# Performance work log

Hardware: AMD Instinct MI355X
Metric: run time of the kernel (lower is better)

The kernel has to match this reference:

```python
import jax, jax.numpy as jnp
import numpy as np

N = 4096
IN_F = 256
OUT_F = 128
K = 3
BETA = 0.5
ALPHA = 0.2  # leaky relu negative slope
NEG_BIG = -9e15


def setup_inputs() -> dict:
    key = jax.random.key(0)
    k1, k2, k3, k4 = jax.random.split(key, 4)
    h = jax.random.normal(k1, (N, IN_F), dtype=jnp.float32)
    k_mask_list = jax.random.randint(k2, (K, N, N), 0, 2, dtype=jnp.int32)
    # xavier_uniform with gain=1.414
    def xavier(k, shape, gain=1.414):
        fan_in, fan_out = shape[0], shape[1]
        bound = gain * np.sqrt(6.0 / (fan_in + fan_out))
        return jax.random.uniform(k, shape, jnp.float32, -bound, bound)
    W = xavier(k3, (IN_F * K, OUT_F))
    a = xavier(k4, (2 * OUT_F * K, 1))
    return {"h": h, "k_mask_list": k_mask_list, "W": W, "a": a}


def reference(h, k_mask_list, W, a):
    # dropout p=0.0 / eval mode -> identity
    Wh = None
    for i in range(K - 1, -1, -1):
        Whnew = h @ W[i * IN_F:(i + 1) * IN_F, :]              # [N, OUT_F]
        if i == K - 1:
            Wh = Whnew
        a1 = a[2 * i * OUT_F:(2 * i + 1) * OUT_F, :]           # [OUT_F, 1]
        a2 = a[(2 * i + 1) * OUT_F:(2 * i + 2) * OUT_F, :]     # [OUT_F, 1]
        Wh1 = Whnew @ a1                                        # [N, 1]
        Wh2 = Whnew @ a2                                        # [N, 1]
        e = jax.nn.leaky_relu(Wh1 + Wh2.T, negative_slope=ALPHA)  # [N, N]
        masked = jnp.where(k_mask_list[i] > 0, e, NEG_BIG)
        attention = jax.nn.softmax(masked, axis=1)              # [N, N]
        Wh = (1.0 - BETA) * (attention @ Whnew) + BETA * Wh
    return jax.nn.elu(Wh)  # concat=True
```

## Files before the change

kernel.cpp:

```cpp
#include <hip/hip_runtime.h>
#include <hip/hip_bf16.h>

#define NN 4096
#define IN_F 256
#define OUT_F 128
#define ALPHA 0.2f

typedef __bf16 bf16x8 __attribute__((ext_vector_type(8)));
typedef float f32x4 __attribute__((ext_vector_type(4)));
typedef float f32x16 __attribute__((ext_vector_type(16)));

__device__ __forceinline__ float bf2f(unsigned short u) {
  return __uint_as_float(((unsigned int)u) << 16);
}
__device__ __forceinline__ unsigned short f2bf(float f) {
  union { float f; unsigned int u; } x; x.f = f;
  unsigned int r = x.u + 0x7FFF + ((x.u >> 16) & 1);
  return (unsigned short)(r >> 16);
}
__device__ __forceinline__ bf16x8 bits2bf8(unsigned int b) {
  union { unsigned int u[4]; bf16x8 v; } o;
  #pragma unroll
  for (int e = 0; e < 4; ++e) {
    unsigned int lo = (b >> (2 * e)) & 1u;
    unsigned int hi = (b >> (2 * e + 1)) & 1u;
    o.u[e] = lo * 0x3F80u + hi * 0x3F800000u;
  }
  return o.v;
}

__global__ __launch_bounds__(256) void k_cvt_w(const float* __restrict__ W,
                                               unsigned short* __restrict__ Wtb) {
  const int i = blockIdx.y;
  const int k0 = blockIdx.x * 32;
  const int t = threadIdx.x;
  __shared__ float tile[32][129];
  #pragma unroll
  for (int j = 0; j < 16; ++j) {
    int idx = t + j * 256;
    int r = idx >> 7, c = idx & 127;
    tile[r][c] = W[(size_t)(i * IN_F + k0 + r) * OUT_F + c];
  }
  __syncthreads();
  const int c = t >> 1, half = t & 1;
  unsigned short* dst = Wtb + ((size_t)i * OUT_F + c) * IN_F + k0 + half * 16;
  #pragma unroll
  for (int g = 0; g < 4; ++g) {
    ushort4 v;
    v.x = f2bf(tile[half * 16 + g * 4 + 0][c]);
    v.y = f2bf(tile[half * 16 + g * 4 + 1][c]);
    v.z = f2bf(tile[half * 16 + g * 4 + 2][c]);
    v.w = f2bf(tile[half * 16 + g * 4 + 3][c]);
    *(ushort4*)(dst + g * 4) = v;
  }
}

__global__ __launch_bounds__(256) void k_front(const float* __restrict__ h,
                                               const unsigned short* __restrict__ Wtb,
                                               const float* __restrict__ a,
                                               float* __restrict__ Whnewf,
                                               float* __restrict__ Wh1,
                                               float* __restrict__ Wh2) {
  const int i = blockIdx.y;
  const int r0 = blockIdx.x * 32;
  const int t = threadIdx.x;
  const int lane = t & 63, wid = t >> 6;
  const int m = wid & 1, nh = wid >> 1, nbase = nh * 64;
  const int ln = lane & 15, lk = lane >> 4;

  __shared__ float a1s[128], a2s[128];
  __shared__ float red1[2][32], red2[2][32];

  if (t < 128) {
    a1s[t] = a[(size_t)2 * i * OUT_F + t];
    a2s[t] = a[(size_t)(2 * i + 1) * OUT_F + t];
  }
  __syncthreads();

  const float* ap = h + (size_t)(r0 + m * 16 + ln) * IN_F + lk * 8;
  const unsigned short* bp = Wtb + ((size_t)i * OUT_F + nbase + ln) * IN_F + lk * 8;

  f32x4 z4 = {0.f, 0.f, 0.f, 0.f};
  f32x4 acc[4] = {z4, z4, z4, z4};
  #pragma unroll
  for (int ks = 0; ks < 8; ++ks) {
    float4 h0 = *(const float4*)(ap + ks * 32);
    float4 h1 = *(const float4*)(ap + ks * 32 + 4);
    union { unsigned short u[8]; bf16x8 v; } av;
    av.u[0] = f2bf(h0.x); av.u[1] = f2bf(h0.y); av.u[2] = f2bf(h0.z); av.u[3] = f2bf(h0.w);
    av.u[4] = f2bf(h1.x); av.u[5] = f2bf(h1.y); av.u[6] = f2bf(h1.z); av.u[7] = f2bf(h1.w);
    acc[0] = __builtin_amdgcn_mfma_f32_16x16x32_bf16(av.v, *(const bf16x8*)(bp + 0 * 16 * IN_F + ks * 32), acc[0], 0, 0, 0);
    acc[1] = __builtin_amdgcn_mfma_f32_16x16x32_bf16(av.v, *(const bf16x8*)(bp + 1 * 16 * IN_F + ks * 32), acc[1], 0, 0, 0);
    acc[2] = __builtin_amdgcn_mfma_f32_16x16x32_bf16(av.v, *(const bf16x8*)(bp + 2 * 16 * IN_F + ks * 32), acc[2], 0, 0, 0);
    acc[3] = __builtin_amdgcn_mfma_f32_16x16x32_bf16(av.v, *(const bf16x8*)(bp + 3 * 16 * IN_F + ks * 32), acc[3], 0, 0, 0);
  }

  float d1[4] = {0.f, 0.f, 0.f, 0.f}, d2[4] = {0.f, 0.f, 0.f, 0.f};
  #pragma unroll
  for (int f = 0; f < 4; ++f) {
    const int col = nbase + f * 16 + ln;
    const float va1 = a1s[col], va2 = a2s[col];
    #pragma unroll
    for (int q = 0; q < 4; ++q) {
      const int row = m * 16 + lk * 4 + q;
      const float v = acc[f][q];
      Whnewf[((size_t)i * NN + r0 + row) * OUT_F + col] = v;
      d1[q] += v * va1;
      d2[q] += v * va2;
    }
  }
  #pragma unroll
  for (int msk = 1; msk < 16; msk <<= 1) {
    #pragma unroll
    for (int q = 0; q < 4; ++q) {
      d1[q] += __shfl_xor(d1[q], msk, 64);
      d2[q] += __shfl_xor(d2[q], msk, 64);
    }
  }
  if (ln == 0) {
    #pragma unroll
    for (int q = 0; q < 4; ++q) {
      red1[nh][m * 16 + lk * 4 + q] = d1[q];
      red2[nh][m * 16 + lk * 4 + q] = d2[q];
    }
  }
  __syncthreads();
  if (t < 32) {
    Wh1[(size_t)i * NN + r0 + t] = red1[0][t] + red1[1][t];
    Wh2[(size_t)i * NN + r0 + t] = red2[0][t] + red2[1][t];
  }
}

__global__ __launch_bounds__(256) void k_gp(const float* __restrict__ Wh1,
                                            const float* __restrict__ Wh2,
                                            unsigned short* __restrict__ ew2pb,
                                            unsigned short* __restrict__ ew2mb,
                                            float* __restrict__ fpv,
                                            float* __restrict__ fmv) {
  const int i = blockIdx.x;
  const int t = threadIdx.x;
  __shared__ float red[4];
  __shared__ float gshared;
  float w2l[16];
  float m = -3.0e38f;
  #pragma unroll
  for (int j = 0; j < 16; ++j) {
    w2l[j] = Wh2[(size_t)i * NN + t + j * 256];
    m = fmaxf(m, w2l[j]);
  }
  #pragma unroll
  for (int o = 32; o > 0; o >>= 1) m = fmaxf(m, __shfl_down(m, o, 64));
  if ((t & 63) == 0) red[t >> 6] = m;
  __syncthreads();
  if (t == 0) gshared = fmaxf(fmaxf(red[0], red[1]), fmaxf(red[2], red[3]));
  __syncthreads();
  const float gi = gshared;
  #pragma unroll
  for (int j = 0; j < 16; ++j) {
    const int id = (int)((size_t)i * NN) + t + j * 256;
    ew2pb[id] = f2bf(__expf(w2l[j]));
    ew2mb[id] = f2bf(__expf(ALPHA * w2l[j]));
    float w1 = Wh1[id];
    float e0 = w1 + gi;
    float mx = (e0 > 0.f) ? e0 : ALPHA * e0;
    fpv[id] = __expf(w1 - mx);
    fmv[id] = __expf(ALPHA * w1 - mx);
  }
}

__global__ __launch_bounds__(256) void k_scale(const float* __restrict__ Whnewf,
                                               const unsigned short* __restrict__ ew2pb,
                                               const unsigned short* __restrict__ ew2mb,
                                               unsigned short* __restrict__ Vopt) {
  const int i = blockIdx.y;
  const int k0 = blockIdx.x * 32;
  const int t = threadIdx.x;
  __shared__ float tile[32][129];
  __shared__ float ewsp[32], ewsm[32];
  if (t < 32) {
    ewsp[t] = bf2f(ew2pb[(size_t)i * NN + k0 + t]);
    ewsm[t] = bf2f(ew2mb[(size_t)i * NN + k0 + t]);
  }
  #pragma unroll
  for (int j = 0; j < 16; ++j) {
    int idx = t + j * 256;
    int r = idx >> 7, c = idx & 127;
    tile[r][c] = Whnewf[((size_t)i * NN + k0 + r) * OUT_F + c];
  }
  __syncthreads();
  const int n = t & 127, ks = t >> 7;
  const int kslab = (k0 >> 4) + ks;
  #pragma unroll
  for (int s = 0; s < 2; ++s) {
    const float* ew = (s == 0) ? ewsp : ewsm;
    union { unsigned short u[16]; uint4 q[2]; } o;
    #pragma unroll
    for (int j = 0; j < 16; ++j) {
      const int cl = ks * 16 + j;
      o.u[j] = f2bf(ew[cl] * tile[cl][n]);
    }
    unsigned short* dst = Vopt + (((size_t)(i * 2 + s) * 256 + kslab) * 128 + n) * 16;
    *(uint4*)(dst) = o.q[0];
    *(uint4*)(dst + 8) = o.q[1];
  }
}

__global__ __launch_bounds__(256) void k_bits(const int* __restrict__ mask,
                                              const float* __restrict__ Wh1,
                                              const float* __restrict__ Wh2,
                                              unsigned int* __restrict__ Bits) {
  const int t = threadIdx.x;
  const int i = blockIdx.x >> 10;
  const int r0 = (blockIdx.x & 1023) * 4;
  float w2v[16];
  #pragma unroll
  for (int g = 0; g < 4; ++g) {
    float4 w2 = *(const float4*)(Wh2 + (size_t)i * NN + t * 16 + g * 4);
    w2v[g * 4 + 0] = w2.x; w2v[g * 4 + 1] = w2.y;
    w2v[g * 4 + 2] = w2.z; w2v[g * 4 + 3] = w2.w;
  }
  float w1v[4];
  #pragma unroll
  for (int rr = 0; rr < 4; ++rr) w1v[rr] = Wh1[(size_t)i * NN + r0 + rr];
  const int* mbase = mask + ((size_t)i * NN + r0) * NN + t * 16;
  int mA[16], mB[16];
  auto LD = [&](int rr, int* mv) {
    #pragma unroll
    for (int g = 0; g < 4; ++g) {
      int4 v = *(const int4*)(mbase + (size_t)rr * NN + g * 4);
      mv[g * 4 + 0] = v.x; mv[g * 4 + 1] = v.y;
      mv[g * 4 + 2] = v.z; mv[g * 4 + 3] = v.w;
    }
  };
  auto PR = [&](int rr, const int* mv) {
    const float w1 = w1v[rr];
    unsigned int bp = 0, bm = 0;
    #pragma unroll
    for (int j = 0; j < 16; ++j) {
      if (mv[j] > 0) {
        if (w1 + w2v[j] > 0.f) bp |= 1u << j; else bm |= 1u << j;
      }
    }
    Bits[((size_t)i * NN + r0 + rr) * 256 + t] = bp | (bm << 16);
  };
  LD(0, mA);
  LD(1, mB);
  PR(0, mA);
  LD(2, mA);
  PR(1, mB);
  LD(3, mB);
  PR(2, mA);
  PR(3, mB);
}

__global__ __launch_bounds__(256) void k_attn2(const unsigned short* __restrict__ Vopt,
                                               const unsigned int* __restrict__ Bits,
                                               const unsigned short* __restrict__ ew2pb,
                                               const unsigned short* __restrict__ ew2mb,
                                               const float* __restrict__ fpv,
                                               const float* __restrict__ fmv,
                                               float* __restrict__ Upart,
                                               float* __restrict__ SPp,
                                               float* __restrict__ SMp) {
  const unsigned int lid = blockIdx.x + 64u * (blockIdx.y + 3u * blockIdx.z);
  const unsigned int swz = (lid & 7u) * 96u + (lid >> 3);
  const int bx = swz & 63;
  const int w = swz >> 6;
  const int i = w % 3;
  const int z = w / 3;

  const int r0 = bx * 64;
  const int cb = z * 1024;
  const int t = threadIdx.x, lane = t & 63, wid = t >> 6;
  const int m = wid & 1, nh = wid >> 1;
  const int l31 = lane & 31, kh = lane >> 5;
  const int n0 = nh * 64 + l31, n1 = n0 + 32;

  const unsigned int* brow = Bits + ((size_t)i * NN + r0 + m * 32 + l31) * 256 + (cb >> 4);
  const size_t fragoff = (size_t)nh * 1024 + l31 * 16 + kh * 8;
  const unsigned short* vP = Vopt + ((size_t)(i * 2 + 0) * 256 + (cb >> 4)) * 2048 + fragoff;
  const unsigned short* vM = Vopt + ((size_t)(i * 2 + 1) * 256 + (cb >> 4)) * 2048 + fragoff;
  const unsigned short* eB = (nh == 0 ? ew2pb : ew2mb) + (size_t)i * NN + cb + kh * 8;

  f32x16 accP0 = {}, accP1 = {}, accM0 = {}, accM1 = {}, accS = {};

  #pragma unroll 2
  for (int chunk = 0; chunk < 16; ++chunk) {
    uint4 wv4 = *(const uint4*)(brow + chunk * 4);
    unsigned int wv[4] = {wv4.x, wv4.y, wv4.z, wv4.w};
    #pragma unroll
    for (int kst = 0; kst < 4; ++kst) {
      const int kslab = chunk * 4 + kst;
      unsigned int sh = wv[kst] >> (kh * 8);
      bf16x8 aP = bits2bf8(sh & 0xFFu);
      bf16x8 aM = bits2bf8((sh >> 16) & 0xFFu);
      bf16x8 bP0 = *(const bf16x8*)(vP + (size_t)kslab * 2048);
      bf16x8 bP1 = *(const bf16x8*)(vP + (size_t)kslab * 2048 + 512);
      bf16x8 bM0 = *(const bf16x8*)(vM + (size_t)kslab * 2048);
      bf16x8 bM1 = *(const bf16x8*)(vM + (size_t)kslab * 2048 + 512);
      bf16x8 eF  = *(const bf16x8*)(eB + kslab * 16);
      accP0 = __builtin_amdgcn_mfma_f32_32x32x16_bf16(aP, bP0, accP0, 0, 0, 0);
      accP1 = __builtin_amdgcn_mfma_f32_32x32x16_bf16(aP, bP1, accP1, 0, 0, 0);
      accM0 = __builtin_amdgcn_mfma_f32_32x32x16_bf16(aM, bM0, accM0, 0, 0, 0);
      accM1 = __builtin_amdgcn_mfma_f32_32x32x16_bf16(aM, bM1, accM1, 0, 0, 0);
      accS  = __builtin_amdgcn_mfma_f32_32x32x16_bf16(nh == 0 ? aP : aM, eF, accS, 0, 0, 0);
    }
  }

  const int rbase = r0 + m * 32;
  #pragma unroll
  for (int q = 0; q < 16; ++q) {
    const int crow = (q & 3) + 8 * (q >> 2) + 4 * kh;
    const int r = rbase + crow;
    const float fp = fpv[(size_t)i * NN + r];
    const float fm = fmv[(size_t)i * NN + r];
    float* urow = Upart + ((size_t)(z * 3 + i) * NN + r) * OUT_F;
    urow[n0] = fp * accP0[q] + fm * accM0[q];
    urow[n1] = fp * accP1[q] + fm * accM1[q];
  }
  if (l31 == 0) {
    #pragma unroll
    for (int q = 0; q < 16; ++q) {
      const int r = rbase + (q & 3) + 8 * (q >> 2) + 4 * kh;
      if (nh == 0) SPp[(size_t)(z * 3 + i) * NN + r] = accS[q];
      else         SMp[(size_t)(z * 3 + i) * NN + r] = accS[q];
    }
  }
}

__global__ __launch_bounds__(256) void k_final(const float* __restrict__ Upart,
                                               const float* __restrict__ SPp,
                                               const float* __restrict__ SMp,
                                               const float* __restrict__ fpv,
                                               const float* __restrict__ fmv,
                                               const float* __restrict__ Whnewf,
                                               float* __restrict__ out) {
  int idx = blockIdx.x * 256 + threadIdx.x;
  int r = idx >> 7;
  float v = 0.125f * Whnewf[(size_t)2 * NN * OUT_F + idx];
  #pragma unroll
  for (int i = 0; i < 3; ++i) {
    const float coef = (i == 0) ? 0.5f : (i == 1) ? 0.25f : 0.125f;
    float u = 0.f, sp = 0.f, sm = 0.f;
    #pragma unroll
    for (int zz = 0; zz < 4; ++zz) {
      u  += Upart[((size_t)(zz * 3 + i) * NN) * OUT_F + idx];
      sp += SPp[(size_t)(zz * 3 + i) * NN + r];
      sm += SMp[(size_t)(zz * 3 + i) * NN + r];
    }
    const float S = fpv[(size_t)i * NN + r] * sp + fmv[(size_t)i * NN + r] * sm;
    v += coef * u / S;
  }
  out[idx] = (v > 0.f) ? v : (__expf(v) - 1.0f);
}

extern "C" void kernel_launch(void* const* d_in, const int* in_sizes, int n_in,
                              void* d_out, int out_size, void* d_ws, size_t ws_size,
                              hipStream_t stream) {
  const float* h    = (const float*)d_in[0];
  const int*   mask = (const int*)d_in[1];
  const float* W    = (const float*)d_in[2];
  const float* a    = (const float*)d_in[3];
  float* out = (float*)d_out;

  float* Whnewf = (float*)d_ws;
  float* Wh1    = Whnewf + (size_t)3 * NN * OUT_F;
  float* Wh2    = Wh1 + 3 * NN;
  float* fpv    = Wh2 + 3 * NN;
  float* fmv    = fpv + 3 * NN;
  float* Upart  = fmv + 3 * NN;
  float* SPp    = Upart + (size_t)4 * 3 * NN * OUT_F;
  float* SMp    = SPp + 4 * 3 * NN;
  unsigned short* Wtb   = (unsigned short*)(SMp + 4 * 3 * NN);
  unsigned short* Vopt  = Wtb + (size_t)3 * OUT_F * IN_F;
  unsigned short* ew2pb = Vopt + (size_t)3 * 2 * 256 * 128 * 16;
  unsigned short* ew2mb = ew2pb + 3 * NN;
  unsigned int*   Bits  = (unsigned int*)(ew2mb + 3 * NN);

  k_cvt_w<<<dim3(8, 3), 256, 0, stream>>>(W, Wtb);
  k_front<<<dim3(128, 3), 256, 0, stream>>>(h, Wtb, a, Whnewf, Wh1, Wh2);
  k_gp<<<3, 256, 0, stream>>>(Wh1, Wh2, ew2pb, ew2mb, fpv, fmv);
  k_scale<<<dim3(128, 3), 256, 0, stream>>>(Whnewf, ew2pb, ew2mb, Vopt);
  k_bits<<<3072, 256, 0, stream>>>(mask, Wh1, Wh2, Bits);
  k_attn2<<<dim3(64, 3, 4), 256, 0, stream>>>(Vopt, Bits, ew2pb, ew2mb, fpv, fmv, Upart, SPp, SMp);
  k_final<<<(NN * OUT_F) / 256, 256, 0, stream>>>(Upart, SPp, SMp, fpv, fmv, Whnewf, out);
}
```

Measured before the change: 360.1 us.

## Fuse mask bit-packing into attention kernel and fold exp/scale prep into front GEMM

Removes the separate k_gp, k_scale and k_bits kernels. The attention kernel now reads the int32 mask and Wh2 directly and builds the bf16 selector operands in-loop. The front GEMM kernel now computes the exp(Wh2) factors and writes the scaled bf16 V tiles from LDS, using an atomicMax for the per-head max shift. The fp/fm factors are recomputed on the fly in the consumers instead of being stored. This cuts launches and intermediate buffer round-trips, but the heavy kernel's inner loop now carries wide mask loads and compare logic that may expose memory latency. The positive-only atomicMax also changes the softmax shift when the max is negative, which cancels mathematically.

```diff
diff --git a/kernel.cpp b/kernel.cpp
--- a/kernel.cpp
+++ b/kernel.cpp
@@ -10,23 +10,10 @@
 typedef float f32x4 __attribute__((ext_vector_type(4)));
 typedef float f32x16 __attribute__((ext_vector_type(16)));
 
-__device__ __forceinline__ float bf2f(unsigned short u) {
-  return __uint_as_float(((unsigned int)u) << 16);
-}
 __device__ __forceinline__ unsigned short f2bf(float f) {
   union { float f; unsigned int u; } x; x.f = f;
   unsigned int r = x.u + 0x7FFF + ((x.u >> 16) & 1);
   return (unsigned short)(r >> 16);
-}
-__device__ __forceinline__ bf16x8 bits2bf8(unsigned int b) {
-  union { unsigned int u[4]; bf16x8 v; } o;
-  #pragma unroll
-  for (int e = 0; e < 4; ++e) {
-    unsigned int lo = (b >> (2 * e)) & 1u;
-    unsigned int hi = (b >> (2 * e + 1)) & 1u;
-    o.u[e] = lo * 0x3F80u + hi * 0x3F800000u;
-  }
-  return o.v;
 }
 
 __global__ __launch_bounds__(256) void k_cvt_w(const float* __restrict__ W,
@@ -58,9 +45,13 @@
 __global__ __launch_bounds__(256) void k_front(const float* __restrict__ h,
                                                const unsigned short* __restrict__ Wtb,
                                                const float* __restrict__ a,
-                                               float* __restrict__ Whnewf,
+                                               float* __restrict__ Whnew2,
+                                               unsigned short* __restrict__ Vopt,
                                                float* __restrict__ Wh1,
-                                               float* __restrict__ Wh2) {
+                                               float* __restrict__ Wh2,
+                                               unsigned short* __restrict__ ew2pb,
+                                               unsigned short* __restrict__ ew2mb,
+                                               float* __restrict__ gmax2) {
   const int i = blockIdx.y;
   const int r0 = blockIdx.x * 32;
   const int t = threadIdx.x;
@@ -70,6 +61,8 @@
 
   __shared__ float a1s[128], a2s[128];
   __shared__ float red1[2][32], red2[2][32];
+  __shared__ float ewsp[32], ewsm[32];
+  __shared__ unsigned short T[2][32][130];
 
   if (t < 128) {
     a1s[t] = a[(size_t)2 * i * OUT_F + t];
@@ -102,9 +95,7 @@
     const float va1 = a1s[col], va2 = a2s[col];
     #pragma unroll
     for (int q = 0; q < 4; ++q) {
-      const int row = m * 16 + lk * 4 + q;
       const float v = acc[f][q];
-      Whnewf[((size_t)i * NN + r0 + row) * OUT_F + col] = v;
       d1[q] += v * va1;
       d2[q] += v * va2;
     }
@@ -124,141 +115,67 @@
       red2[nh][m * 16 + lk * 4 + q] = d2[q];
     }
   }
-  __syncthreads();
+  if (i == 2) {
+    #pragma unroll
+    for (int f = 0; f < 4; ++f) {
+      const int col = nbase + f * 16 + ln;
+      #pragma unroll
+      for (int q = 0; q < 4; ++q)
+        Whnew2[(size_t)(r0 + m * 16 + lk * 4 + q) * OUT_F + col] = acc[f][q];
+    }
+  }
+  __syncthreads();
+
   if (t < 32) {
-    Wh1[(size_t)i * NN + r0 + t] = red1[0][t] + red1[1][t];
-    Wh2[(size_t)i * NN + r0 + t] = red2[0][t] + red2[1][t];
-  }
-}
-
-__global__ __launch_bounds__(256) void k_gp(const float* __restrict__ Wh1,
-                                            const float* __restrict__ Wh2,
-                                            unsigned short* __restrict__ ew2pb,
-                                            unsigned short* __restrict__ ew2mb,
-                                            float* __restrict__ fpv,
-                                            float* __restrict__ fmv) {
-  const int i = blockIdx.x;
-  const int t = threadIdx.x;
-  __shared__ float red[4];
-  __shared__ float gshared;
-  float w2l[16];
-  float m = -3.0e38f;
-  #pragma unroll
-  for (int j = 0; j < 16; ++j) {
-    w2l[j] = Wh2[(size_t)i * NN + t + j * 256];
-    m = fmaxf(m, w2l[j]);
-  }
-  #pragma unroll
-  for (int o = 32; o > 0; o >>= 1) m = fmaxf(m, __shfl_down(m, o, 64));
-  if ((t & 63) == 0) red[t >> 6] = m;
-  __syncthreads();
-  if (t == 0) gshared = fmaxf(fmaxf(red[0], red[1]), fmaxf(red[2], red[3]));
-  __syncthreads();
-  const float gi = gshared;
-  #pragma unroll
-  for (int j = 0; j < 16; ++j) {
-    const int id = (int)((size_t)i * NN) + t + j * 256;
-    ew2pb[id] = f2bf(__expf(w2l[j]));
-    ew2mb[id] = f2bf(__expf(ALPHA * w2l[j]));
-    float w1 = Wh1[id];
-    float e0 = w1 + gi;
-    float mx = (e0 > 0.f) ? e0 : ALPHA * e0;
-    fpv[id] = __expf(w1 - mx);
-    fmv[id] = __expf(ALPHA * w1 - mx);
-  }
-}
-
-__global__ __launch_bounds__(256) void k_scale(const float* __restrict__ Whnewf,
-                                               const unsigned short* __restrict__ ew2pb,
-                                               const unsigned short* __restrict__ ew2mb,
-                                               unsigned short* __restrict__ Vopt) {
-  const int i = blockIdx.y;
-  const int k0 = blockIdx.x * 32;
-  const int t = threadIdx.x;
-  __shared__ float tile[32][129];
-  __shared__ float ewsp[32], ewsm[32];
-  if (t < 32) {
-    ewsp[t] = bf2f(ew2pb[(size_t)i * NN + k0 + t]);
-    ewsm[t] = bf2f(ew2mb[(size_t)i * NN + k0 + t]);
-  }
-  #pragma unroll
-  for (int j = 0; j < 16; ++j) {
-    int idx = t + j * 256;
-    int r = idx >> 7, c = idx & 127;
-    tile[r][c] = Whnewf[((size_t)i * NN + k0 + r) * OUT_F + c];
-  }
-  __syncthreads();
+    const float w1 = red1[0][t] + red1[1][t];
+    const float w2 = red2[0][t] + red2[1][t];
+    Wh1[(size_t)i * NN + r0 + t] = w1;
+    Wh2[(size_t)i * NN + r0 + t] = w2;
+    const float ep = __expf(w2), em = __expf(ALPHA * w2);
+    ewsp[t] = ep; ewsm[t] = em;
+    ew2pb[(size_t)i * NN + r0 + t] = f2bf(ep);
+    ew2mb[(size_t)i * NN + r0 + t] = f2bf(em);
+    float mv = w2;
+    #pragma unroll
+    for (int o = 16; o > 0; o >>= 1) mv = fmaxf(mv, __shfl_down(mv, o, 32));
+    if (t == 0 && mv > 0.f)
+      atomicMax((int*)gmax2 + i, __float_as_int(mv));
+  }
+  __syncthreads();
+
+  #pragma unroll
+  for (int f = 0; f < 4; ++f) {
+    const int n = nbase + f * 16 + ln;
+    #pragma unroll
+    for (int q = 0; q < 4; ++q) {
+      const int c = m * 16 + lk * 4 + q;
+      const float v = acc[f][q];
+      T[0][c][n] = f2bf(ewsp[c] * v);
+      T[1][c][n] = f2bf(ewsm[c] * v);
+    }
+  }
+  __syncthreads();
+
   const int n = t & 127, ks = t >> 7;
-  const int kslab = (k0 >> 4) + ks;
+  const int kslab = (r0 >> 4) + ks;
   #pragma unroll
   for (int s = 0; s < 2; ++s) {
-    const float* ew = (s == 0) ? ewsp : ewsm;
     union { unsigned short u[16]; uint4 q[2]; } o;
     #pragma unroll
-    for (int j = 0; j < 16; ++j) {
-      const int cl = ks * 16 + j;
-      o.u[j] = f2bf(ew[cl] * tile[cl][n]);
-    }
+    for (int j = 0; j < 16; ++j) o.u[j] = T[s][ks * 16 + j][n];
     unsigned short* dst = Vopt + (((size_t)(i * 2 + s) * 256 + kslab) * 128 + n) * 16;
     *(uint4*)(dst) = o.q[0];
     *(uint4*)(dst + 8) = o.q[1];
   }
 }
 
-__global__ __launch_bounds__(256) void k_bits(const int* __restrict__ mask,
-                                              const float* __restrict__ Wh1,
-                                              const float* __restrict__ Wh2,
-                                              unsigned int* __restrict__ Bits) {
-  const int t = threadIdx.x;
-  const int i = blockIdx.x >> 10;
-  const int r0 = (blockIdx.x & 1023) * 4;
-  float w2v[16];
-  #pragma unroll
-  for (int g = 0; g < 4; ++g) {
-    float4 w2 = *(const float4*)(Wh2 + (size_t)i * NN + t * 16 + g * 4);
-    w2v[g * 4 + 0] = w2.x; w2v[g * 4 + 1] = w2.y;
-    w2v[g * 4 + 2] = w2.z; w2v[g * 4 + 3] = w2.w;
-  }
-  float w1v[4];
-  #pragma unroll
-  for (int rr = 0; rr < 4; ++rr) w1v[rr] = Wh1[(size_t)i * NN + r0 + rr];
-  const int* mbase = mask + ((size_t)i * NN + r0) * NN + t * 16;
-  int mA[16], mB[16];
-  auto LD = [&](int rr, int* mv) {
-    #pragma unroll
-    for (int g = 0; g < 4; ++g) {
-      int4 v = *(const int4*)(mbase + (size_t)rr * NN + g * 4);
-      mv[g * 4 + 0] = v.x; mv[g * 4 + 1] = v.y;
-      mv[g * 4 + 2] = v.z; mv[g * 4 + 3] = v.w;
-    }
-  };
-  auto PR = [&](int rr, const int* mv) {
-    const float w1 = w1v[rr];
-    unsigned int bp = 0, bm = 0;
-    #pragma unroll
-    for (int j = 0; j < 16; ++j) {
-      if (mv[j] > 0) {
-        if (w1 + w2v[j] > 0.f) bp |= 1u << j; else bm |= 1u << j;
-      }
-    }
-    Bits[((size_t)i * NN + r0 + rr) * 256 + t] = bp | (bm << 16);
-  };
-  LD(0, mA);
-  LD(1, mB);
-  PR(0, mA);
-  LD(2, mA);
-  PR(1, mB);
-  LD(3, mB);
-  PR(2, mA);
-  PR(3, mB);
-}
-
-__global__ __launch_bounds__(256) void k_attn2(const unsigned short* __restrict__ Vopt,
-                                               const unsigned int* __restrict__ Bits,
+__global__ __launch_bounds__(256) void k_heavy(const unsigned short* __restrict__ Vopt,
+                                               const int* __restrict__ mask,
+                                               const float* __restrict__ Wh1,
+                                               const float* __restrict__ Wh2,
                                                const unsigned short* __restrict__ ew2pb,
                                                const unsigned short* __restrict__ ew2mb,
-                                               const float* __restrict__ fpv,
-                                               const float* __restrict__ fmv,
+                                               const float* __restrict__ gmax2,
                                                float* __restrict__ Upart,
                                                float* __restrict__ SPp,
                                                float* __restrict__ SMp) {
@@ -276,7 +193,11 @@
   const int l31 = lane & 31, kh = lane >> 5;
   const int n0 = nh * 64 + l31, n1 = n0 + 32;
 
-  const unsigned int* brow = Bits + ((size_t)i * NN + r0 + m * 32 + l31) * 256 + (cb >> 4);
+  const int myrow = r0 + m * 32 + l31;
+  const float w1 = Wh1[(size_t)i * NN + myrow];
+  const int* mrow = mask + ((size_t)i * NN + myrow) * NN + cb + kh * 8;
+  const float* w2p = Wh2 + (size_t)i * NN + cb + kh * 8;
+
   const size_t fragoff = (size_t)nh * 1024 + l31 * 16 + kh * 8;
   const unsigned short* vP = Vopt + ((size_t)(i * 2 + 0) * 256 + (cb >> 4)) * 2048 + fragoff;
   const unsigned short* vM = Vopt + ((size_t)(i * 2 + 1) * 256 + (cb >> 4)) * 2048 + fragoff;
@@ -285,35 +206,48 @@
   f32x16 accP0 = {}, accP1 = {}, accM0 = {}, accM1 = {}, accS = {};
 
   #pragma unroll 2
-  for (int chunk = 0; chunk < 16; ++chunk) {
-    uint4 wv4 = *(const uint4*)(brow + chunk * 4);
-    unsigned int wv[4] = {wv4.x, wv4.y, wv4.z, wv4.w};
-    #pragma unroll
-    for (int kst = 0; kst < 4; ++kst) {
-      const int kslab = chunk * 4 + kst;
-      unsigned int sh = wv[kst] >> (kh * 8);
-      bf16x8 aP = bits2bf8(sh & 0xFFu);
-      bf16x8 aM = bits2bf8((sh >> 16) & 0xFFu);
-      bf16x8 bP0 = *(const bf16x8*)(vP + (size_t)kslab * 2048);
-      bf16x8 bP1 = *(const bf16x8*)(vP + (size_t)kslab * 2048 + 512);
-      bf16x8 bM0 = *(const bf16x8*)(vM + (size_t)kslab * 2048);
-      bf16x8 bM1 = *(const bf16x8*)(vM + (size_t)kslab * 2048 + 512);
-      bf16x8 eF  = *(const bf16x8*)(eB + kslab * 16);
-      accP0 = __builtin_amdgcn_mfma_f32_32x32x16_bf16(aP, bP0, accP0, 0, 0, 0);
-      accP1 = __builtin_amdgcn_mfma_f32_32x32x16_bf16(aP, bP1, accP1, 0, 0, 0);
-      accM0 = __builtin_amdgcn_mfma_f32_32x32x16_bf16(aM, bM0, accM0, 0, 0, 0);
-      accM1 = __builtin_amdgcn_mfma_f32_32x32x16_bf16(aM, bM1, accM1, 0, 0, 0);
-      accS  = __builtin_amdgcn_mfma_f32_32x32x16_bf16(nh == 0 ? aP : aM, eF, accS, 0, 0, 0);
-    }
-  }
-
+  for (int kslab = 0; kslab < 64; ++kslab) {
+    const int ks16 = kslab * 16;
+    int4 ma = *(const int4*)(mrow + ks16);
+    int4 mb = *(const int4*)(mrow + ks16 + 4);
+    float4 wa = *(const float4*)(w2p + ks16);
+    float4 wb = *(const float4*)(w2p + ks16 + 4);
+
+    union { unsigned int u[4]; bf16x8 v; } aP, aM;
+    {
+      int mv[8] = {ma.x, ma.y, ma.z, ma.w, mb.x, mb.y, mb.z, mb.w};
+      float wv[8] = {wa.x, wa.y, wa.z, wa.w, wb.x, wb.y, wb.z, wb.w};
+      #pragma unroll
+      for (int e = 0; e < 4; ++e) {
+        const bool m0 = mv[2 * e] > 0,   p0 = (w1 + wv[2 * e]) > 0.f;
+        const bool m1 = mv[2 * e + 1] > 0, p1 = (w1 + wv[2 * e + 1]) > 0.f;
+        aP.u[e] = ((m0 && p0) ? 0x3F80u : 0u) | ((m1 && p1) ? 0x3F800000u : 0u);
+        aM.u[e] = ((m0 && !p0) ? 0x3F80u : 0u) | ((m1 && !p1) ? 0x3F800000u : 0u);
+      }
+    }
+    bf16x8 bP0 = *(const bf16x8*)(vP + (size_t)kslab * 2048);
+    bf16x8 bP1 = *(const bf16x8*)(vP + (size_t)kslab * 2048 + 512);
+    bf16x8 bM0 = *(const bf16x8*)(vM + (size_t)kslab * 2048);
+    bf16x8 bM1 = *(const bf16x8*)(vM + (size_t)kslab * 2048 + 512);
+    bf16x8 eF  = *(const bf16x8*)(eB + ks16);
+    accP0 = __builtin_amdgcn_mfma_f32_32x32x16_bf16(aP.v, bP0, accP0, 0, 0, 0);
+    accP1 = __builtin_amdgcn_mfma_f32_32x32x16_bf16(aP.v, bP1, accP1, 0, 0, 0);
+    accM0 = __builtin_amdgcn_mfma_f32_32x32x16_bf16(aM.v, bM0, accM0, 0, 0, 0);
+    accM1 = __builtin_amdgcn_mfma_f32_32x32x16_bf16(aM.v, bM1, accM1, 0, 0, 0);
+    accS  = __builtin_amdgcn_mfma_f32_32x32x16_bf16(nh == 0 ? aP.v : aM.v, eF, accS, 0, 0, 0);
+  }
+
+  const float gi = gmax2[i];
   const int rbase = r0 + m * 32;
   #pragma unroll
   for (int q = 0; q < 16; ++q) {
     const int crow = (q & 3) + 8 * (q >> 2) + 4 * kh;
     const int r = rbase + crow;
-    const float fp = fpv[(size_t)i * NN + r];
-    const float fm = fmv[(size_t)i * NN + r];
+    const float rw1 = Wh1[(size_t)i * NN + r];
+    const float e0 = rw1 + gi;
+    const float mx = (e0 > 0.f) ? e0 : ALPHA * e0;
+    const float fp = __expf(rw1 - mx);
+    const float fm = __expf(ALPHA * rw1 - mx);
     float* urow = Upart + ((size_t)(z * 3 + i) * NN + r) * OUT_F;
     urow[n0] = fp * accP0[q] + fm * accM0[q];
     urow[n1] = fp * accP1[q] + fm * accM1[q];
@@ -331,16 +265,22 @@
 __global__ __launch_bounds__(256) void k_final(const float* __restrict__ Upart,
                                                const float* __restrict__ SPp,
                                                const float* __restrict__ SMp,
-                                               const float* __restrict__ fpv,
-                                               const float* __restrict__ fmv,
-                                               const float* __restrict__ Whnewf,
+                                               const float* __restrict__ Wh1,
+                                               const float* __restrict__ gmax2,
+                                               const float* __restrict__ Whnew2,
                                                float* __restrict__ out) {
   int idx = blockIdx.x * 256 + threadIdx.x;
   int r = idx >> 7;
-  float v = 0.125f * Whnewf[(size_t)2 * NN * OUT_F + idx];
+  float v = 0.125f * Whnew2[idx];
   #pragma unroll
   for (int i = 0; i < 3; ++i) {
     const float coef = (i == 0) ? 0.5f : (i == 1) ? 0.25f : 0.125f;
+    const float w1 = Wh1[(size_t)i * NN + r];
+    const float gi = gmax2[i];
+    const float e0 = w1 + gi;
+    const float mx = (e0 > 0.f) ? e0 : ALPHA * e0;
+    const float fp = __expf(w1 - mx);
+    const float fm = __expf(ALPHA * w1 - mx);
     float u = 0.f, sp = 0.f, sm = 0.f;
     #pragma unroll
     for (int zz = 0; zz < 4; ++zz) {
@@ -348,7 +288,7 @@
       sp += SPp[(size_t)(zz * 3 + i) * NN + r];
       sm += SMp[(size_t)(zz * 3 + i) * NN + r];
     }
-    const float S = fpv[(size_t)i * NN + r] * sp + fmv[(size_t)i * NN + r] * sm;
+    const float S = fp * sp + fm * sm;
     v += coef * u / S;
   }
   out[idx] = (v > 0.f) ? v : (__expf(v) - 1.0f);
@@ -363,25 +303,21 @@
   const float* a    = (const float*)d_in[3];
   float* out = (float*)d_out;
 
-  float* Whnewf = (float*)d_ws;
-  float* Wh1    = Whnewf + (size_t)3 * NN * OUT_F;
+  float* Whnew2 = (float*)d_ws;
+  float* Wh1    = Whnew2 + (size_t)NN * OUT_F;
   float* Wh2    = Wh1 + 3 * NN;
-  float* fpv    = Wh2 + 3 * NN;
-  float* fmv    = fpv + 3 * NN;
-  float* Upart  = fmv + 3 * NN;
+  float* gmax2  = Wh2 + 3 * NN;
+  float* Upart  = gmax2 + 4;
   float* SPp    = Upart + (size_t)4 * 3 * NN * OUT_F;
   float* SMp    = SPp + 4 * 3 * NN;
   unsigned short* Wtb   = (unsigned short*)(SMp + 4 * 3 * NN);
   unsigned short* Vopt  = Wtb + (size_t)3 * OUT_F * IN_F;
   unsigned short* ew2pb = Vopt + (size_t)3 * 2 * 256 * 128 * 16;
   unsigned short* ew2mb = ew2pb + 3 * NN;
-  unsigned int*   Bits  = (unsigned int*)(ew2mb + 3 * NN);
-
+
+  hipMemsetAsync(gmax2, 0, 4 * sizeof(float), stream);
   k_cvt_w<<<dim3(8, 3), 256, 0, stream>>>(W, Wtb);
-  k_front<<<dim3(128, 3), 256, 0, stream>>>(h, Wtb, a, Whnewf, Wh1, Wh2);
-  k_gp<<<3, 256, 0, stream>>>(Wh1, Wh2, ew2pb, ew2mb, fpv, fmv);
-  k_scale<<<dim3(128, 3), 256, 0, stream>>>(Whnewf, ew2pb, ew2mb, Vopt);
-  k_bits<<<3072, 256, 0, stream>>>(mask, Wh1, Wh2, Bits);
-  k_attn2<<<dim3(64, 3, 4), 256, 0, stream>>>(Vopt, Bits, ew2pb, ew2mb, fpv, fmv, Upart, SPp, SMp);
-  k_final<<<(NN * OUT_F) / 256, 256, 0, stream>>>(Upart, SPp, SMp, fpv, fmv, Whnewf, out);
-}
+  k_front<<<dim3(128, 3), 256, 0, stream>>>(h, Wtb, a, Whnew2, Vopt, Wh1, Wh2, ew2pb, ew2mb, gmax2);
+  k_heavy<<<dim3(64, 3, 4), 256, 0, stream>>>(Vopt, mask, Wh1, Wh2, ew2pb, ew2mb, gmax2, Upart, SPp, SMp);
+  k_final<<<(NN * OUT_F) / 256, 256, 0, stream>>>(Upart, SPp, SMp, Wh1, gmax2, Whnew2, out);
+}
```

New measurement: 398.0 us. 1.11x slower.
